# Kernel optimization log

Hardware: AMD Instinct MI355X
Metric: run time of the kernel (lower is better)

Reference implementation:

```python
import jax, jax.numpy as jnp
import numpy as np

_B, _F, _H, _W = 4, 256, 64, 64
_C, _S = 19, 256  # num_classes, memory-bank half size


def setup_inputs() -> dict:
    key = jax.random.key(0)
    k1, k2, k3, k4, k5 = jax.random.split(key, 5)
    memory_bank = jax.random.normal(k1, (_C, 2 * _S, _F), dtype=jnp.float32)
    pred_rep = jax.random.normal(k2, (_B, _F, _H, _W), dtype=jnp.float32)
    labels = jax.random.randint(k3, (_B, _H, _W), 0, _C)
    mask = jax.random.randint(k4, (_B, _H, _W), 0, 2).astype(bool)
    which_memory = jax.random.randint(k5, (_B, _H, _W), 0, 2)
    return {
        "memory_bank": memory_bank,
        "pred_rep": pred_rep,
        "labels": labels,
        "mask": mask,
        "which_memory": which_memory,
        "num_classes": _C,
    }


def reference(memory_bank, pred_rep, labels, mask, which_memory, num_classes, temp=0.5):
    eps = 1e-12
    C, twoS, F = memory_bank.shape
    S = twoS // 2
    # pixels-first layout: [P, F]
    feats = jnp.transpose(pred_rep, (0, 2, 3, 1)).reshape(-1, F)
    lab = labels.reshape(-1)
    msk = mask.reshape(-1)
    wm = which_memory.reshape(-1)
    mem = memory_bank.reshape(-1, F)  # [C*2S, F]
    fn = jnp.linalg.norm(feats, axis=1)  # [P]
    mn = jnp.linalg.norm(mem, axis=1)    # [C*2S]
    cos = (feats @ mem.T) / (fn[:, None] * mn[None, :])
    E = jnp.exp(cos / temp)              # [P, C*2S]
    Eb = E.reshape(-1, C, twoS)
    total = Eb.sum(axis=(1, 2))          # [P] sum over full bank
    block_sum = Eb.sum(axis=2)           # [P, C]
    loss = jnp.float32(0.0)
    class_count = jnp.float32(0.0)
    for i in range(num_classes):
        choice = msk & (lab == i)
        cnt = choice.sum()
        down = total - block_sum[:, i]   # negatives = all other classes
        block = Eb[:, i, :]              # [P, 2S] positives for class i
        contrib = jnp.float32(0.0)
        for net in range(2):
            sel = choice & (wm == 1 - net)
            pos = block[:, :S] if net == 0 else block[:, S:]
            term = -jnp.log(pos / (pos + down[:, None] + eps) + eps)
            contrib = contrib + jnp.where(sel[:, None], term, 0.0).sum()
        denom = jnp.maximum(cnt, 1).astype(jnp.float32) * S
        loss = loss + jnp.where(cnt > 0, contrib / denom, 0.0)
        class_count = class_count + (cnt > 0).astype(jnp.float32)
    return loss / jnp.maximum(class_count, 1.0)
```

## Files before the change

### kernel.cpp

```cpp
#include <hip/hip_runtime.h>
#include <hip/hip_bf16.h>
#include <math.h>

#define B_ 4
#define F_ 256
#define C_ 19
#define S_ 256
#define N_ 16384
#define M_ 9728
#define MT_ 38
#define NP_ 18816
#define PREP_PRED 256
#define PREP_BUCKET0 2688
#define GEMM_BLKS 512
#define P2_BLOCKS (C_ * 16)

typedef __bf16 bf16_t;
typedef bf16_t bf16x8 __attribute__((ext_vector_type(8)));
typedef float floatx4 __attribute__((ext_vector_type(4)));

#define AS1 __attribute__((address_space(1)))
#define AS3 __attribute__((address_space(3)))

__device__ inline size_t fragoff(int row, int f) {
    return ((size_t)((row >> 4) * 8 + (f >> 5))) * 512
         + (size_t)((((f >> 3) & 3) * 128) + ((row & 15) * 8) + (f & 7));
}

__global__ __launch_bounds__(256) void k_prep(const float* __restrict__ pred,
                                              const float* __restrict__ mem,
                                              __hip_bfloat16* __restrict__ A16f,
                                              __hip_bfloat16* __restrict__ B16,
                                              const int* __restrict__ labels,
                                              const int* __restrict__ mask,
                                              int* __restrict__ ccnt,
                                              int* __restrict__ pix) {
    int bid = blockIdx.x;
    int t = threadIdx.x;
    if (bid < PREP_PRED) {
        __shared__ float part[4][64];
        __shared__ float invf_s[64];
        int b = bid >> 6, hw0 = (bid & 63) * 64;
        int j = t & 63, q = t >> 6;
        int n0 = b * 4096 + hw0;

        const float* base = pred + ((size_t)b * F_ + q * 64) * 4096 + hw0 + j;
        float v[64];
        float s = 0.f;
        #pragma unroll
        for (int i = 0; i < 64; ++i) {
            float x = base[(size_t)i * 4096];
            v[i] = x;
            s += x * x;
        }
        part[q][j] = s;
        __syncthreads();
        if (t < 64) invf_s[t] = 1.0f / sqrtf(part[0][t] + part[1][t] + part[2][t] + part[3][t]);
        __syncthreads();
        float invf = invf_s[j];
        #pragma unroll
        for (int c = 0; c < 8; ++c) {
            int f = q * 64 + c * 8;
            __hip_bfloat16 tmp[8];
            #pragma unroll
            for (int u = 0; u < 8; ++u) tmp[u] = __float2bfloat16(v[c * 8 + u] * invf);
            *(float4*)&A16f[fragoff(n0 + j, f)] = *(float4*)tmp;
        }
    } else if (bid < PREP_BUCKET0) {
        int row  = (bid - PREP_PRED) * 4 + (t >> 6);
        int lane = t & 63;
        float4 a = ((const float4*)(mem + (size_t)row * F_))[lane];
        float s = a.x*a.x + a.y*a.y + a.z*a.z + a.w*a.w;
        #pragma unroll
        for (int off = 32; off; off >>= 1) s += __shfl_xor(s, off, 64);
        float invm = 1.0f / sqrtf(s);
        __hip_bfloat16 tmp[4];
        tmp[0] = __float2bfloat16(a.x * invm);
        tmp[1] = __float2bfloat16(a.y * invm);
        tmp[2] = __float2bfloat16(a.z * invm);
        tmp[3] = __float2bfloat16(a.w * invm);
        *(float2*)&B16[fragoff(row, lane * 4)] = *(float2*)tmp;
    } else {
        __shared__ int hist[C_], base_s[C_], cur[C_];
        int n0 = (bid - PREP_BUCKET0) * 256;
        if (t < C_) { hist[t] = 0; cur[t] = 0; }
        __syncthreads();
        int myc = labels[n0 + t];
        int mym = mask[n0 + t];
        if (mym) atomicAdd(&hist[myc], 1);
        __syncthreads();
        if (t < C_) base_s[t] = atomicAdd(&ccnt[t], hist[t]);
        __syncthreads();
        if (mym) {
            int o = atomicAdd(&cur[myc], 1);
            pix[myc * N_ + base_s[myc] + o] = n0 + t;
        }
    }
}

__global__ __launch_bounds__(256) void k_compact(const __hip_bfloat16* __restrict__ A16f,
                                                 const int* __restrict__ ccnt,
                                                 const int* __restrict__ pix,
                                                 __hip_bfloat16* __restrict__ A16c) {
    __shared__ int pidx_s[64];
    int bid = blockIdx.x, t = threadIdx.x;
    int slot0 = bid * 64;
    int slot = slot0 + (t & 63);
    int run = 0, pixid = 0;
    #pragma unroll
    for (int cc = 0; cc < C_; ++cc) {
        int cn = ccnt[cc];
        if (slot >= run && slot < run + cn) pixid = pix[cc * N_ + slot - run];
        run += (cn + 127) & ~127;
    }
    if (slot0 >= run) return;
    if (t < 64) pidx_s[t] = pixid;
    __syncthreads();
    #pragma unroll
    for (int s = 0; s < 8; ++s) {
        int k = t + 256 * s;
        int row = ((k >> 9) << 4) | (k & 15);
        int f   = ((k >> 6) & 7) * 32 + ((k >> 4) & 3) * 8;
        float4 v = *(const float4*)&A16f[fragoff(pidx_s[row], f)];
        *(float4*)&A16c[((size_t)slot0 << 8) + (size_t)k * 8] = v;
    }
}

__global__ __launch_bounds__(512, 4) void k_pass1(const __hip_bfloat16* __restrict__ A16c,
                                                  const __hip_bfloat16* __restrict__ B16,
                                                  const int* __restrict__ ccnt,
                                                  float* __restrict__ totpart) {
    __shared__ __hip_bfloat16 As[128 * 256];
    __shared__ float totals_s[2][4][128];
    int bid = blockIdx.x;
    int t = threadIdx.x;
    int w = t >> 6, lane = t & 63;
    int nh = w & 1, mq = w >> 1;

    int padded_total = 0;
    #pragma unroll
    for (int cc = 0; cc < C_; ++cc) padded_total += (ccnt[cc] + 127) & ~127;
    int nt_total = padded_total >> 7;
    if (nt_total == 0) return;
    int nchunk = GEMM_BLKS / nt_total;
    if (nchunk > MT_) nchunk = MT_;
    if (nchunk < 1) nchunk = 1;
    if (bid >= nt_total * nchunk) return;
    int panel = bid % nt_total;
    int chunk = bid / nt_total;
    int slot0 = panel << 7;

    {
        const __hip_bfloat16* src = A16c + ((size_t)slot0 << 8) + w * 4096 + lane * 8;
        __hip_bfloat16* dst = &As[w * 4096];
        #pragma unroll
        for (int i = 0; i < 8; ++i)
            __builtin_amdgcn_global_load_lds((const AS1 unsigned int*)(src + i * 512),
                                             (AS3 unsigned int*)(dst + i * 512), 16, 0, 0);
    }
    __syncthreads();

    int colL = lane & 15, rgrp = (lane >> 4) * 4;
    int p = 0;
    for (int mt = chunk; mt < MT_; mt += nchunk, p ^= 1) {
        floatx4 acc[4][4];
        #pragma unroll
        for (int i = 0; i < 4; ++i)
            #pragma unroll
            for (int j2 = 0; j2 < 4; ++j2) acc[i][j2] = (floatx4){0.f, 0.f, 0.f, 0.f};

        const bf16x8* Bp = (const bf16x8*)B16 + ((size_t)(mt * 16 + mq * 4) * 8) * 64 + lane;

        #pragma unroll
        for (int kt = 0; kt < 8; ++kt) {
            bf16x8 af[4], bfr[4];
            #pragma unroll
            for (int ni = 0; ni < 4; ++ni)
                af[ni] = *(const bf16x8*)&As[((nh * 4 + ni) * 8 + kt) * 512 + lane * 8];
            #pragma unroll
            for (int mi = 0; mi < 4; ++mi)
                bfr[mi] = Bp[(size_t)(mi * 8 + kt) * 64];
            __builtin_amdgcn_s_setprio(1);
            #pragma unroll
            for (int ni = 0; ni < 4; ++ni)
                #pragma unroll
                for (int mi = 0; mi < 4; ++mi)
                    acc[ni][mi] = __builtin_amdgcn_mfma_f32_16x16x32_bf16(af[ni], bfr[mi], acc[ni][mi], 0, 0, 0);
            __builtin_amdgcn_s_setprio(0);
        }

        float racc[4][4];
        #pragma unroll
        for (int ni = 0; ni < 4; ++ni)
            #pragma unroll
            for (int r = 0; r < 4; ++r) racc[ni][r] = 0.f;
        #pragma unroll
        for (int ni = 0; ni < 4; ++ni)
            #pragma unroll
            for (int mi = 0; mi < 4; ++mi)
                #pragma unroll
                for (int r = 0; r < 4; ++r)
                    racc[ni][r] += __expf(2.0f * acc[ni][mi][r]);

        #pragma unroll
        for (int ni = 0; ni < 4; ++ni)
            #pragma unroll
            for (int r = 0; r < 4; ++r) {
                float s = racc[ni][r];
                s += __shfl_xor(s, 1, 64);
                s += __shfl_xor(s, 2, 64);
                s += __shfl_xor(s, 4, 64);
                s += __shfl_xor(s, 8, 64);
                if (colL == 0) totals_s[p][mq][nh * 64 + ni * 16 + rgrp + r] = s;
            }
        asm volatile("s_waitcnt lgkmcnt(0)\n\ts_barrier" ::: "memory");
        if (t < 128)
            totpart[(size_t)mt * NP_ + slot0 + t] =
                totals_s[p][0][t] + totals_s[p][1][t] + totals_s[p][2][t] + totals_s[p][3][t];
    }
}

__global__ __launch_bounds__(512) void k_pass2(const __hip_bfloat16* __restrict__ A16c,
                                               const __hip_bfloat16* __restrict__ B16,
                                               const int* __restrict__ ccnt,
                                               const int* __restrict__ pix,
                                               const float* __restrict__ totpart,
                                               const int* __restrict__ wmem,
                                               float* __restrict__ class_sum,
                                               int* __restrict__ done,
                                               float* __restrict__ out) {
    __shared__ __hip_bfloat16 As[64 * 256];
    __shared__ float tot_s[64];
    __shared__ int wm_s[64];
    __shared__ float bsum_s[8][64];
    __shared__ float wsum_s[8][64];
    __shared__ float down_s[64];
    __shared__ float term_s[64];

    int c = blockIdx.x, tile = blockIdx.y;
    int cnt = ccnt[c];
    int t = threadIdx.x, ws = t >> 6, lane = t & 63;

    if (tile * 64 >= cnt) {
        if (t == 0) {
            __threadfence();
            int old = atomicAdd(done, 1);
            if (old == P2_BLOCKS - 1) {
                float loss = 0.f, kc = 0.f;
                for (int cc = 0; cc < C_; ++cc) {
                    int cn = ccnt[cc];
                    float sc = atomicAdd(&class_sum[cc], 0.f);
                    if (cn > 0) { loss += sc / ((float)cn * (float)S_); kc += 1.f; }
                }
                out[0] = loss / fmaxf(kc, 1.f);
            }
        }
        return;
    }

    int pre = 0;
    #pragma unroll
    for (int cc = 0; cc < C_; ++cc) if (cc < c) pre += (ccnt[cc] + 127) & ~127;
    int slot0 = pre + tile * 64;

    {
        const __hip_bfloat16* src = A16c + ((size_t)slot0 << 8) + t * 8;
        __hip_bfloat16* dst = &As[t * 8];
        #pragma unroll
        for (int i = 0; i < 4; ++i)
            __builtin_amdgcn_global_load_lds((const AS1 unsigned int*)(src + i * 4096),
                                             (AS3 unsigned int*)(dst + i * 4096), 16, 0, 0);
    }

    if (t < 64) {
        int i = tile * 64 + t;
        int p = pix[c * N_ + (i < cnt ? i : 0)];
        wm_s[t] = wmem[p];
    }

    {
        int px = t >> 3, g = t & 7;
        float s = 0.f;
        for (int i = g; i < MT_; i += 8) s += totpart[(size_t)i * NP_ + slot0 + px];
        s += __shfl_xor(s, 1, 64);
        s += __shfl_xor(s, 2, 64);
        s += __shfl_xor(s, 4, 64);
        if (g == 0) tot_s[px] = s;
    }
    __syncthreads();

    floatx4 acc[4][4];
    #pragma unroll
    for (int i = 0; i < 4; ++i)
        #pragma unroll
        for (int j = 0; j < 4; ++j) acc[i][j] = (floatx4){0.f, 0.f, 0.f, 0.f};

    const bf16x8* Bp = (const bf16x8*)B16 + ((size_t)(c * 32 + ws * 4) * 8) * 64 + lane;
    #pragma unroll
    for (int kt = 0; kt < 8; ++kt) {
        bf16x8 af[4], bfr[4];
        #pragma unroll
        for (int ni = 0; ni < 4; ++ni)
            af[ni] = *(const bf16x8*)&As[(ni * 8 + kt) * 512 + lane * 8];
        #pragma unroll
        for (int mi = 0; mi < 4; ++mi) bfr[mi] = Bp[(size_t)(mi * 8 + kt) * 64];
        #pragma unroll
        for (int ni = 0; ni < 4; ++ni)
            #pragma unroll
            for (int mi = 0; mi < 4; ++mi)
                acc[ni][mi] = __builtin_amdgcn_mfma_f32_16x16x32_bf16(af[ni], bfr[mi], acc[ni][mi], 0, 0, 0);
    }

    int colL = lane & 15, rgrp = (lane >> 4) * 4;
    float Ev[4][4][4];
    #pragma unroll
    for (int ni = 0; ni < 4; ++ni)
        #pragma unroll
        for (int mi = 0; mi < 4; ++mi)
            #pragma unroll
            for (int r = 0; r < 4; ++r)
                Ev[ni][mi][r] = __expf(2.0f * acc[ni][mi][r]);

    #pragma unroll
    for (int ni = 0; ni < 4; ++ni)
        #pragma unroll
        for (int r = 0; r < 4; ++r) {
            float s = Ev[ni][0][r] + Ev[ni][1][r] + Ev[ni][2][r] + Ev[ni][3][r];
            s += __shfl_xor(s, 1, 64);
            s += __shfl_xor(s, 2, 64);
            s += __shfl_xor(s, 4, 64);
            s += __shfl_xor(s, 8, 64);
            if (colL == 0) bsum_s[ws][ni * 16 + rgrp + r] = s;
        }
    __syncthreads();
    if (t < 64) {
        float bs = 0.f;
        #pragma unroll
        for (int w2 = 0; w2 < 8; ++w2) bs += bsum_s[w2][t];
        down_s[t] = tot_s[t] - bs;
    }
    __syncthreads();

    #pragma unroll
    for (int ni = 0; ni < 4; ++ni)
        #pragma unroll
        for (int r = 0; r < 4; ++r) {
            int row = ni * 16 + rgrp + r;
            bool sel = (wm_s[row] == 1) ? (ws < 4) : (ws >= 4);
            float tt = 0.f;
            if (sel) {
                float dwn = down_s[row];
                #pragma unroll
                for (int mi = 0; mi < 4; ++mi) {
                    float pv = Ev[ni][mi][r];
                    tt += -logf(pv / (pv + dwn + 1e-12f) + 1e-12f);
                }
            }
            tt += __shfl_xor(tt, 1, 64);
            tt += __shfl_xor(tt, 2, 64);
            tt += __shfl_xor(tt, 4, 64);
            tt += __shfl_xor(tt, 8, 64);
            if (colL == 0) wsum_s[ws][row] = tt;
        }
    __syncthreads();
    if (t < 64) {
        int i = tile * 64 + t;
        float s = 0.f;
        if (i < cnt) {
            #pragma unroll
            for (int w2 = 0; w2 < 8; ++w2) s += wsum_s[w2][t];
        }
        term_s[t] = s;
    }
    __syncthreads();
    if (t < 64) {
        float s = term_s[t];
        #pragma unroll
        for (int off = 1; off < 64; off <<= 1) s += __shfl_xor(s, off, 64);
        if (t == 0) {
            atomicAdd(&class_sum[c], s);
            __threadfence();
            int old = atomicAdd(done, 1);
            if (old == P2_BLOCKS - 1) {
                float loss = 0.f, kc = 0.f;
                for (int cc = 0; cc < C_; ++cc) {
                    int cn = ccnt[cc];
                    float sc = atomicAdd(&class_sum[cc], 0.f);
                    if (cn > 0) { loss += sc / ((float)cn * (float)S_); kc += 1.f; }
                }
                out[0] = loss / fmaxf(kc, 1.f);
            }
        }
    }
}

extern "C" void kernel_launch(void* const* d_in, const int* in_sizes, int n_in,
                              void* d_out, int out_size, void* d_ws, size_t ws_size,
                              hipStream_t stream) {
    const float* mem    = (const float*)d_in[0];
    const float* pred   = (const float*)d_in[1];
    const int*   labels = (const int*)  d_in[2];
    const int*   mask   = (const int*)  d_in[3];
    const int*   wmem   = (const int*)  d_in[4];
    float* out = (float*)d_out;

    float* ws = (float*)d_ws;
    float* totpart   = ws;
    int*   ctrl      = (int*)(ws + 715008);
    int*   ccnt      = ctrl;
    float* class_sum = (float*)(ctrl + 19);
    int*   done      = ctrl + 38;
    int*   pix       = (int*)(ws + 715048);
    __hip_bfloat16* A16f = (__hip_bfloat16*)(ws + 1026344);
    __hip_bfloat16* A16c = (__hip_bfloat16*)(ws + 3123496);
    __hip_bfloat16* B16  = (__hip_bfloat16*)(ws + 5531944);

    hipMemsetAsync(ctrl, 0, 40 * sizeof(int), stream);

    k_prep<<<PREP_BUCKET0 + 64, 256, 0, stream>>>(pred, mem, A16f, B16,
                                                  labels, mask, ccnt, pix);

    k_compact<<<NP_ / 64, 256, 0, stream>>>(A16f, ccnt, pix, A16c);

    k_pass1<<<GEMM_BLKS, 512, 0, stream>>>(A16c, B16, ccnt, totpart);

    dim3 g2(C_, 16);
    k_pass2<<<g2, 512, 0, stream>>>(A16c, B16, ccnt, pix, totpart, wmem,
                                    class_sum, done, out);
}
```

Before: 176.3 us.

## Scatter normalized pixel features directly into compacted class-bucket layout

Bucketing of pixels by class now runs as its own small kernel first and records each pixel's (class, position) in a slot map. The prep kernel then writes normalized bf16 features straight into the compacted per-class buffer, so the full-size intermediate array and the separate gather/compact kernel are no longer needed. This removes one kernel launch and a full bf16 write-then-read round trip. In exchange, the bucket kernel must finish before prep can start, and masked-out pixels skip their writes.

```diff
diff --git a/kernel.cpp b/kernel.cpp
--- a/kernel.cpp
+++ b/kernel.cpp
@@ -11,7 +11,7 @@
 #define MT_ 38
 #define NP_ 18816
 #define PREP_PRED 256
-#define PREP_BUCKET0 2688
+#define PREP_TOTAL 2688
 #define GEMM_BLKS 512
 #define P2_BLOCKS (C_ * 16)
 
@@ -27,22 +27,53 @@
          + (size_t)((((f >> 3) & 3) * 128) + ((row & 15) * 8) + (f & 7));
 }
 
+__global__ __launch_bounds__(256) void k_bucket(const int* __restrict__ labels,
+                                                const int* __restrict__ mask,
+                                                int* __restrict__ ccnt,
+                                                int* __restrict__ pix,
+                                                int* __restrict__ slotmap) {
+    __shared__ int hist[C_], base_s[C_], cur[C_];
+    int t = threadIdx.x;
+    int n0 = blockIdx.x * 256;
+    if (t < C_) { hist[t] = 0; cur[t] = 0; }
+    __syncthreads();
+    int myc = labels[n0 + t];
+    int mym = mask[n0 + t];
+    if (mym) atomicAdd(&hist[myc], 1);
+    __syncthreads();
+    if (t < C_) base_s[t] = atomicAdd(&ccnt[t], hist[t]);
+    __syncthreads();
+    int sm = -1;
+    if (mym) {
+        int o = atomicAdd(&cur[myc], 1);
+        int pos = base_s[myc] + o;
+        pix[myc * N_ + pos] = n0 + t;
+        sm = (myc << 16) | pos;
+    }
+    slotmap[n0 + t] = sm;
+}
+
 __global__ __launch_bounds__(256) void k_prep(const float* __restrict__ pred,
                                               const float* __restrict__ mem,
-                                              __hip_bfloat16* __restrict__ A16f,
+                                              __hip_bfloat16* __restrict__ A16c,
                                               __hip_bfloat16* __restrict__ B16,
-                                              const int* __restrict__ labels,
-                                              const int* __restrict__ mask,
-                                              int* __restrict__ ccnt,
-                                              int* __restrict__ pix) {
+                                              const int* __restrict__ ccnt,
+                                              const int* __restrict__ slotmap) {
     int bid = blockIdx.x;
     int t = threadIdx.x;
     if (bid < PREP_PRED) {
         __shared__ float part[4][64];
         __shared__ float invf_s[64];
+        __shared__ int pre_s[C_];
         int b = bid >> 6, hw0 = (bid & 63) * 64;
         int j = t & 63, q = t >> 6;
         int n0 = b * 4096 + hw0;
+
+        if (t < C_) {
+            int pre = 0;
+            for (int cc = 0; cc < t; ++cc) pre += (ccnt[cc] + 127) & ~127;
+            pre_s[t] = pre;
+        }
 
         const float* base = pred + ((size_t)b * F_ + q * 64) * 4096 + hw0 + j;
         float v[64];
@@ -57,16 +88,20 @@
         __syncthreads();
         if (t < 64) invf_s[t] = 1.0f / sqrtf(part[0][t] + part[1][t] + part[2][t] + part[3][t]);
         __syncthreads();
-        float invf = invf_s[j];
-        #pragma unroll
-        for (int c = 0; c < 8; ++c) {
-            int f = q * 64 + c * 8;
-            __hip_bfloat16 tmp[8];
-            #pragma unroll
-            for (int u = 0; u < 8; ++u) tmp[u] = __float2bfloat16(v[c * 8 + u] * invf);
-            *(float4*)&A16f[fragoff(n0 + j, f)] = *(float4*)tmp;
-        }
-    } else if (bid < PREP_BUCKET0) {
+        int sm = slotmap[n0 + j];
+        if (sm >= 0) {
+            int slot = pre_s[sm >> 16] + (sm & 0xffff);
+            float invf = invf_s[j];
+            #pragma unroll
+            for (int c = 0; c < 8; ++c) {
+                int f = q * 64 + c * 8;
+                __hip_bfloat16 tmp[8];
+                #pragma unroll
+                for (int u = 0; u < 8; ++u) tmp[u] = __float2bfloat16(v[c * 8 + u] * invf);
+                *(float4*)&A16c[fragoff(slot, f)] = *(float4*)tmp;
+            }
+        }
+    } else {
         int row  = (bid - PREP_PRED) * 4 + (t >> 6);
         int lane = t & 63;
         float4 a = ((const float4*)(mem + (size_t)row * F_))[lane];
@@ -80,49 +115,6 @@
         tmp[2] = __float2bfloat16(a.z * invm);
         tmp[3] = __float2bfloat16(a.w * invm);
         *(float2*)&B16[fragoff(row, lane * 4)] = *(float2*)tmp;
-    } else {
-        __shared__ int hist[C_], base_s[C_], cur[C_];
-        int n0 = (bid - PREP_BUCKET0) * 256;
-        if (t < C_) { hist[t] = 0; cur[t] = 0; }
-        __syncthreads();
-        int myc = labels[n0 + t];
-        int mym = mask[n0 + t];
-        if (mym) atomicAdd(&hist[myc], 1);
-        __syncthreads();
-        if (t < C_) base_s[t] = atomicAdd(&ccnt[t], hist[t]);
-        __syncthreads();
-        if (mym) {
-            int o = atomicAdd(&cur[myc], 1);
-            pix[myc * N_ + base_s[myc] + o] = n0 + t;
-        }
-    }
-}
-
-__global__ __launch_bounds__(256) void k_compact(const __hip_bfloat16* __restrict__ A16f,
-                                                 const int* __restrict__ ccnt,
-                                                 const int* __restrict__ pix,
-                                                 __hip_bfloat16* __restrict__ A16c) {
-    __shared__ int pidx_s[64];
-    int bid = blockIdx.x, t = threadIdx.x;
-    int slot0 = bid * 64;
-    int slot = slot0 + (t & 63);
-    int run = 0, pixid = 0;
-    #pragma unroll
-    for (int cc = 0; cc < C_; ++cc) {
-        int cn = ccnt[cc];
-        if (slot >= run && slot < run + cn) pixid = pix[cc * N_ + slot - run];
-        run += (cn + 127) & ~127;
-    }
-    if (slot0 >= run) return;
-    if (t < 64) pidx_s[t] = pixid;
-    __syncthreads();
-    #pragma unroll
-    for (int s = 0; s < 8; ++s) {
-        int k = t + 256 * s;
-        int row = ((k >> 9) << 4) | (k & 15);
-        int f   = ((k >> 6) & 7) * 32 + ((k >> 4) & 3) * 8;
-        float4 v = *(const float4*)&A16f[fragoff(pidx_s[row], f)];
-        *(float4*)&A16c[((size_t)slot0 << 8) + (size_t)k * 8] = v;
     }
 }
 
@@ -411,16 +403,15 @@
     float* class_sum = (float*)(ctrl + 19);
     int*   done      = ctrl + 38;
     int*   pix       = (int*)(ws + 715048);
-    __hip_bfloat16* A16f = (__hip_bfloat16*)(ws + 1026344);
-    __hip_bfloat16* A16c = (__hip_bfloat16*)(ws + 3123496);
-    __hip_bfloat16* B16  = (__hip_bfloat16*)(ws + 5531944);
+    int*   slotmap   = (int*)(ws + 1026344);
+    __hip_bfloat16* A16c = (__hip_bfloat16*)(ws + 1042728);
+    __hip_bfloat16* B16  = (__hip_bfloat16*)(ws + 3451176);
 
     hipMemsetAsync(ctrl, 0, 40 * sizeof(int), stream);
 
-    k_prep<<<PREP_BUCKET0 + 64, 256, 0, stream>>>(pred, mem, A16f, B16,
-                                                  labels, mask, ccnt, pix);
-
-    k_compact<<<NP_ / 64, 256, 0, stream>>>(A16f, ccnt, pix, A16c);
+    k_bucket<<<N_ / 256, 256, 0, stream>>>(labels, mask, ccnt, pix, slotmap);
+
+    k_prep<<<PREP_TOTAL, 256, 0, stream>>>(pred, mem, A16c, B16, ccnt, slotmap);
 
     k_pass1<<<GEMM_BLKS, 512, 0, stream>>>(A16c, B16, ccnt, totpart);
 
```

Result: faster. 171.9 us (-2.5%).
